# Kernel tuning notes

Measured on AMD Instinct MI355X. Metric: run time of the kernel, lower is better.

Reference implementation:

```python
import jax, jax.numpy as jnp
import numpy as np

B, S, DM, H, DK, DV = 2, 2048, 1024, 16, 64, 64

def setup_inputs() -> dict:
    key = jax.random.key(0)
    ks = jax.random.split(key, 12)
    s = 0.02
    return {
        "Q": jax.random.normal(ks[0], (B, S, DM), jnp.float32),
        "K": jax.random.normal(ks[1], (B, S, DM), jnp.float32),
        "V": jax.random.normal(ks[2], (B, S, DM), jnp.float32),
        "mask": jax.random.randint(ks[3], (B, S, S), 0, 2).astype(bool),
        "wq": jax.random.normal(ks[4], (DM, H * DK), jnp.float32) * s,
        "bq": jnp.zeros((H * DK,), jnp.float32),
        "wk": jax.random.normal(ks[5], (DM, H * DK), jnp.float32) * s,
        "bk": jnp.zeros((H * DK,), jnp.float32),
        "wv": jax.random.normal(ks[6], (DM, H * DV), jnp.float32) * s,
        "bv": jnp.zeros((H * DV,), jnp.float32),
        "wo": jax.random.normal(ks[7], (H * DV, DM), jnp.float32) * s,
        "bo": jnp.zeros((DM,), jnp.float32),
    }

def reference(Q, K, V, mask, wq, bq, wk, bk, wv, bv, wo, bo):
    b = Q.shape[0]
    # projections -> [b, h, s, d]
    q = (Q @ wq + bq).reshape(b, -1, H, DK).transpose(0, 2, 1, 3)
    k = (K @ wk + bk).reshape(b, -1, H, DK).transpose(0, 2, 1, 3)
    v = (V @ wv + bv).reshape(b, -1, H, DV).transpose(0, 2, 1, 3)
    # scaled dot-product attention with boolean mask (True = masked out)
    scores = jnp.einsum("bhqd,bhkd->bhqk", q, k) / jnp.sqrt(jnp.float32(DK))
    scores = jnp.where(mask[:, None, :, :], jnp.float32(-1e9), scores)
    attn = jax.nn.softmax(scores, axis=-1)  # [b,h,s,s]
    ctx = jnp.einsum("bhqk,bhkd->bhqd", attn, v)
    ctx = ctx.transpose(0, 2, 1, 3).reshape(b, -1, H * DV)
    out = ctx @ wo + bo  # [b, s, d_model]
    return out, attn
```

## Files before the change

### kernel.cpp

```cpp
#include <hip/hip_runtime.h>

typedef unsigned short u16;
typedef unsigned int u32;
typedef unsigned long long u64;
typedef __attribute__((ext_vector_type(8))) short bf16x8;
typedef __attribute__((ext_vector_type(4))) float f32x4;

#define NB 2
#define NS 2048
#define NDM 1024
#define NH 16

#define MFMA_B16(a, b, c) __builtin_amdgcn_mfma_f32_16x16x32_bf16(a, b, c, 0, 0, 0)

__device__ __forceinline__ u16 f2bf(float f) {
  union { float f; unsigned u; } v; v.f = f;
  return (u16)((v.u + 0x7fffu + ((v.u >> 16) & 1u)) >> 16);
}
__device__ __forceinline__ float bf2f(u16 h) {
  union { float f; unsigned u; } v; v.u = ((u32)h) << 16; return v.f;
}

__global__ __launch_bounds__(256) void cast3_bf16(const float* __restrict__ a,
                                                  const float* __restrict__ b,
                                                  const float* __restrict__ c,
                                                  u16* __restrict__ oa, u16* __restrict__ ob,
                                                  u16* __restrict__ oc) {
  int i = blockIdx.x * 256 + threadIdx.x;
  const float* src; u16* dst; int j;
  if (i < 1048576) { src = a; dst = oa; j = i; }
  else if (i < 2097152) { src = b; dst = ob; j = i - 1048576; }
  else { src = c; dst = oc; j = i - 2097152; }
  const float4 v = reinterpret_cast<const float4*>(src)[j];
  ushort4 o; o.x = f2bf(v.x); o.y = f2bf(v.y); o.z = f2bf(v.z); o.w = f2bf(v.w);
  reinterpret_cast<ushort4*>(dst)[j] = o;
}

struct TW4 { const float* in[4]; u16* out[4]; };
__global__ __launch_bounds__(256) void transpose_w4(TW4 tw) {
  __shared__ float tile[32][33];
  const float* in = tw.in[blockIdx.z];
  u16* out = tw.out[blockIdx.z];
  int bx = blockIdx.x, by = blockIdx.y;
  int x = threadIdx.x & 31, y0 = threadIdx.x >> 5;
#pragma unroll
  for (int i = 0; i < 4; i++) {
    int y = y0 + i * 8;
    tile[y][x] = in[(by * 32 + y) * NDM + bx * 32 + x];
  }
  __syncthreads();
#pragma unroll
  for (int i = 0; i < 4; i++) {
    int y = y0 + i * 8;
    out[(bx * 32 + y) * NDM + by * 32 + x] = f2bf(tile[x][y]);
  }
}

__global__ __launch_bounds__(256) void mask2bits(const u32* __restrict__ mask, u32* __restrict__ mb) {
  int idx = blockIdx.x * 256 + threadIdx.x;
  u32 mw0 = mask[threadIdx.x & 63];
  bool floatmode = (__ballot(mw0 == 0x3F800000u) != 0ull);
  bool bytemode = !floatmode && (__ballot((mw0 >> 8) != 0u) != 0ull);
  int row = idx >> 6;
  int wword = idx & 63;
  u32 bits = 0;
  if (!bytemode) {
    const uint4* p = reinterpret_cast<const uint4*>(mask + (size_t)row * 2048 + wword * 32);
#pragma unroll
    for (int i = 0; i < 8; i++) {
      uint4 v = p[i];
      bits |= (v.x ? 1u : 0u) << (i * 4 + 0);
      bits |= (v.y ? 1u : 0u) << (i * 4 + 1);
      bits |= (v.z ? 1u : 0u) << (i * 4 + 2);
      bits |= (v.w ? 1u : 0u) << (i * 4 + 3);
    }
  } else {
    const uint4* p = reinterpret_cast<const uint4*>(
        reinterpret_cast<const unsigned char*>(mask) + (size_t)row * 2048 + wword * 32);
#pragma unroll
    for (int i = 0; i < 2; i++) {
      uint4 v = p[i];
      u32 wsv[4] = {v.x, v.y, v.z, v.w};
#pragma unroll
      for (int j = 0; j < 4; j++)
#pragma unroll
        for (int kq = 0; kq < 4; kq++)
          bits |= ((((wsv[j] >> (kq * 8)) & 0xffu) != 0u) ? 1u : 0u) << (i * 16 + j * 4 + kq);
    }
  }
  mb[idx] = bits;
}

struct GArgs { const u16* X; const u16* W; const float* bias; void* out; int mode; float scale; };

__global__ __launch_bounds__(256, 2) void gemm_bt(GArgs g0, GArgs g1, GArgs g2) {
  GArgs ga = (blockIdx.z == 0) ? g0 : (blockIdx.z == 1 ? g1 : g2);
  const int K = 1024, N = 1024;
  __shared__ u16 As[128 * 32];
  __shared__ u16 Bs[128 * 32];
  const int t = threadIdx.x, w = t >> 6, l = t & 63;
  const int m0 = blockIdx.x * 128, n0 = blockIdx.y * 128;
  const int wm = (w >> 1) * 64, wn = (w & 1) * 64;
  const f32x4 fz = {0.f, 0.f, 0.f, 0.f};
  f32x4 acc[4][4];
#pragma unroll
  for (int i = 0; i < 4; i++)
#pragma unroll
    for (int j = 0; j < 4; j++) acc[i][j] = fz;

  for (int k0 = 0; k0 < K; k0 += 32) {
#pragma unroll
    for (int i = 0; i < 2; i++) {
      int idx = i * 256 + w * 64 + l;
      int r = idx >> 2, c = (idx & 3) * 8;
      __builtin_amdgcn_global_load_lds(
          reinterpret_cast<const unsigned*>(ga.X + (size_t)(m0 + r) * K + k0 + c),
          reinterpret_cast<unsigned*>(&As[(i * 256 + w * 64) * 8]), 16, 0, 0);
      __builtin_amdgcn_global_load_lds(
          reinterpret_cast<const unsigned*>(ga.W + (size_t)(n0 + r) * K + k0 + c),
          reinterpret_cast<unsigned*>(&Bs[(i * 256 + w * 64) * 8]), 16, 0, 0);
    }
    __syncthreads();
    bf16x8 af[4], bfr[4];
#pragma unroll
    for (int mt = 0; mt < 4; mt++)
      af[mt] = *reinterpret_cast<const bf16x8*>(&As[(wm + mt * 16 + (l & 15)) * 32 + (l >> 4) * 8]);
#pragma unroll
    for (int nt = 0; nt < 4; nt++)
      bfr[nt] = *reinterpret_cast<const bf16x8*>(&Bs[(wn + nt * 16 + (l & 15)) * 32 + (l >> 4) * 8]);
#pragma unroll
    for (int mt = 0; mt < 4; mt++)
#pragma unroll
      for (int nt = 0; nt < 4; nt++)
        acc[mt][nt] = MFMA_B16(af[mt], bfr[nt], acc[mt][nt]);
    __syncthreads();
  }

#pragma unroll
  for (int nt = 0; nt < 4; nt++) {
    int n = n0 + wn + nt * 16 + (l & 15);
    float bias = ga.bias[n];
#pragma unroll
    for (int mt = 0; mt < 4; mt++) {
      int mb = m0 + wm + mt * 16 + ((l >> 4) << 2);
#pragma unroll
      for (int r = 0; r < 4; r++) {
        int m = mb + r;
        float v = (acc[mt][nt][r] + bias) * ga.scale;
        if (ga.mode == 2) {
          reinterpret_cast<float*>(ga.out)[(size_t)m * N + n] = v;
        } else {
          int b = m >> 11, s = m & 2047, h = n >> 6, d = n & 63;
          if (ga.mode == 0)
            reinterpret_cast<u16*>(ga.out)[(((size_t)(b * NH + h) * NS + s) << 6) + d] = f2bf(v);
          else
            reinterpret_cast<u16*>(ga.out)[((size_t)(b * NH + h) * 64 + d) * NS + s] = f2bf(v);
        }
      }
    }
  }
}

__global__ __launch_bounds__(256, 4) void attn_kernel(
    const u16* __restrict__ qh, const u16* __restrict__ kh, const u16* __restrict__ vT,
    const u32* __restrict__ mb, float* __restrict__ attn, u16* __restrict__ ctx) {
  __shared__ u16 Ks[2][32 * 64];
  __shared__ u16 Vs[2][64 * 32];
  __shared__ u16 Ps[4][16 * 40];
  const int tid = threadIdx.x, w = tid >> 6, l = tid & 63;
  int id = blockIdx.x;
  int wgid = (id & 7) * 128 + (id >> 3);
  int qt = wgid & 31, pr = wgid >> 5;
  int h = pr & 15, b = pr >> 4;
  const size_t head = (size_t)b * NH + h;
  const u16* qp = qh + head * NS * 64;
  const u16* kp = kh + head * NS * 64;
  const u16* vp = vT + head * 64 * NS;
  const int qr0 = qt * 64 + w * 16;
  const int lo = l & 15, hi = l >> 4;
  const int rbase = hi << 2;
  const f32x4 fz = {0.f, 0.f, 0.f, 0.f};

  bf16x8 aq0, aq1;
  {
    const u16* p = qp + (size_t)(qr0 + lo) * 64 + hi * 8;
    aq0 = *reinterpret_cast<const bf16x8*>(p);
    aq1 = *reinterpret_cast<const bf16x8*>(p + 32);
  }
  const u32* mrow = mb + ((size_t)b * NS + qr0 + rbase) * 64;

  const int k_row = tid >> 3, k_slot = tid & 7;
  const u16* ksrc0 = kp + (size_t)k_row * 64 + ((k_slot ^ (k_row & 7)) * 8);
  const int v_dv = tid >> 2, v_slot = tid & 3;
  const u16* vsrc0 = vp + (size_t)v_dv * NS + ((v_slot ^ ((v_dv >> 1) & 3)) * 8);
  const int sxk = lo & 7;
  const int sxv = (lo >> 1) & 3;

#define STAGE_KT(tt)                                                                    \
  __builtin_amdgcn_global_load_lds(                                                     \
      reinterpret_cast<const unsigned*>(ksrc0 + (size_t)(tt) * 2048),                   \
      reinterpret_cast<unsigned*>(&Ks[(tt) & 1][w * 512]), 16, 0, 0);
#define STAGE_VT(tt)                                                                    \
  __builtin_amdgcn_global_load_lds(                                                     \
      reinterpret_cast<const unsigned*>(vsrc0 + (size_t)(tt) * 32),                     \
      reinterpret_cast<unsigned*>(&Vs[(tt) & 1][w * 512]), 16, 0, 0);

  float rs0 = 0.f, rs1 = 0.f, rs2 = 0.f, rs3 = 0.f;

  u32 mc0 = mrow[0], mc1 = mrow[64], mc2 = mrow[128], mc3 = mrow[192];
  STAGE_KT(0);
  asm volatile("s_waitcnt vmcnt(0)" ::: "memory");
  __builtin_amdgcn_s_barrier();
  asm volatile("" ::: "memory");

  for (int t = 0; t < 64; ++t) {
    STAGE_KT(t + 1);
    u32 mn0 = mrow[t + 1], mn1 = mrow[65 + t], mn2 = mrow[129 + t], mn3 = mrow[193 + t];
    asm volatile("" ::: "memory");
    const u16* kbase = &Ks[t & 1][0];
    bf16x8 b00 = *reinterpret_cast<const bf16x8*>(&kbase[(lo) * 64 + ((hi ^ sxk) * 8)]);
    bf16x8 b01 = *reinterpret_cast<const bf16x8*>(&kbase[(lo) * 64 + (((4 + hi) ^ sxk) * 8)]);
    bf16x8 b10 = *reinterpret_cast<const bf16x8*>(&kbase[(16 + lo) * 64 + ((hi ^ sxk) * 8)]);
    bf16x8 b11 = *reinterpret_cast<const bf16x8*>(&kbase[(16 + lo) * 64 + (((4 + hi) ^ sxk) * 8)]);
    f32x4 s0 = MFMA_B16(aq1, b01, MFMA_B16(aq0, b00, fz));
    f32x4 s1 = MFMA_B16(aq1, b11, MFMA_B16(aq0, b10, fz));
    rs0 += ((mc0 >> lo) & 1u) ? 0.f : __expf(s0[0]);
    rs1 += ((mc1 >> lo) & 1u) ? 0.f : __expf(s0[1]);
    rs2 += ((mc2 >> lo) & 1u) ? 0.f : __expf(s0[2]);
    rs3 += ((mc3 >> lo) & 1u) ? 0.f : __expf(s0[3]);
    int bit1 = 16 + lo;
    rs0 += ((mc0 >> bit1) & 1u) ? 0.f : __expf(s1[0]);
    rs1 += ((mc1 >> bit1) & 1u) ? 0.f : __expf(s1[1]);
    rs2 += ((mc2 >> bit1) & 1u) ? 0.f : __expf(s1[2]);
    rs3 += ((mc3 >> bit1) & 1u) ? 0.f : __expf(s1[3]);
    mc0 = mn0; mc1 = mn1; mc2 = mn2; mc3 = mn3;
    asm volatile("s_waitcnt vmcnt(4)" ::: "memory");
    __builtin_amdgcn_s_barrier();
    asm volatile("" ::: "memory");
  }

  {
    float v;
    v = rs0; v += __shfl_xor(v, 1); v += __shfl_xor(v, 2); v += __shfl_xor(v, 4); v += __shfl_xor(v, 8);
    rs0 = 1.f / fmaxf(v, 1e-30f);
    v = rs1; v += __shfl_xor(v, 1); v += __shfl_xor(v, 2); v += __shfl_xor(v, 4); v += __shfl_xor(v, 8);
    rs1 = 1.f / fmaxf(v, 1e-30f);
    v = rs2; v += __shfl_xor(v, 1); v += __shfl_xor(v, 2); v += __shfl_xor(v, 4); v += __shfl_xor(v, 8);
    rs2 = 1.f / fmaxf(v, 1e-30f);
    v = rs3; v += __shfl_xor(v, 1); v += __shfl_xor(v, 2); v += __shfl_xor(v, 4); v += __shfl_xor(v, 8);
    rs3 = 1.f / fmaxf(v, 1e-30f);
  }

  f32x4 c0 = fz, c1 = fz, c2 = fz, c3 = fz;
  float* abase = attn + (head * NS + qr0) * NS;
  u16* psw = &Ps[w][0];
  const int srow = l >> 2, schunk = l & 3;

  mc0 = mrow[0]; mc1 = mrow[64]; mc2 = mrow[128]; mc3 = mrow[192];
  STAGE_KT(0);
  STAGE_VT(0);
  asm volatile("s_waitcnt vmcnt(0)" ::: "memory");
  __builtin_amdgcn_s_barrier();
  asm volatile("" ::: "memory");

  for (int t = 0; t < 64; ++t) {
    STAGE_KT(t + 1);
    STAGE_VT(t + 1);
    u32 mn0 = mrow[t + 1], mn1 = mrow[65 + t], mn2 = mrow[129 + t], mn3 = mrow[193 + t];
    asm volatile("" ::: "memory");
    const u16* kbase = &Ks[t & 1][0];
    const u16* vbase = &Vs[t & 1][0];
    bf16x8 b00 = *reinterpret_cast<const bf16x8*>(&kbase[(lo) * 64 + ((hi ^ sxk) * 8)]);
    bf16x8 b01 = *reinterpret_cast<const bf16x8*>(&kbase[(lo) * 64 + (((4 + hi) ^ sxk) * 8)]);
    bf16x8 b10 = *reinterpret_cast<const bf16x8*>(&kbase[(16 + lo) * 64 + ((hi ^ sxk) * 8)]);
    bf16x8 b11 = *reinterpret_cast<const bf16x8*>(&kbase[(16 + lo) * 64 + (((4 + hi) ^ sxk) * 8)]);
    f32x4 s0 = MFMA_B16(aq1, b01, MFMA_B16(aq0, b00, fz));
    f32x4 s1 = MFMA_B16(aq1, b11, MFMA_B16(aq0, b10, fz));
    float p;
    p = ((mc0 >> lo) & 1u) ? 0.f : __expf(s0[0]) * rs0; psw[(rbase + 0) * 40 + lo] = f2bf(p);
    p = ((mc1 >> lo) & 1u) ? 0.f : __expf(s0[1]) * rs1; psw[(rbase + 1) * 40 + lo] = f2bf(p);
    p = ((mc2 >> lo) & 1u) ? 0.f : __expf(s0[2]) * rs2; psw[(rbase + 2) * 40 + lo] = f2bf(p);
    p = ((mc3 >> lo) & 1u) ? 0.f : __expf(s0[3]) * rs3; psw[(rbase + 3) * 40 + lo] = f2bf(p);
    int bit1 = 16 + lo;
    p = ((mc0 >> bit1) & 1u) ? 0.f : __expf(s1[0]) * rs0; psw[(rbase + 0) * 40 + 16 + lo] = f2bf(p);
    p = ((mc1 >> bit1) & 1u) ? 0.f : __expf(s1[1]) * rs1; psw[(rbase + 1) * 40 + 16 + lo] = f2bf(p);
    p = ((mc2 >> bit1) & 1u) ? 0.f : __expf(s1[2]) * rs2; psw[(rbase + 2) * 40 + 16 + lo] = f2bf(p);
    p = ((mc3 >> bit1) & 1u) ? 0.f : __expf(s1[3]) * rs3; psw[(rbase + 3) * 40 + 16 + lo] = f2bf(p);
    mc0 = mn0; mc1 = mn1; mc2 = mn2; mc3 = mn3;
    {
      bf16x8 pa = *reinterpret_cast<const bf16x8*>(&psw[lo * 40 + hi * 8]);
      bf16x8 v0 = *reinterpret_cast<const bf16x8*>(&vbase[(lo) * 32 + ((hi ^ sxv) * 8)]);
      bf16x8 v1 = *reinterpret_cast<const bf16x8*>(&vbase[(16 + lo) * 32 + ((hi ^ sxv) * 8)]);
      bf16x8 v2 = *reinterpret_cast<const bf16x8*>(&vbase[(32 + lo) * 32 + ((hi ^ sxv) * 8)]);
      bf16x8 v3 = *reinterpret_cast<const bf16x8*>(&vbase[(48 + lo) * 32 + ((hi ^ sxv) * 8)]);
      c0 = MFMA_B16(pa, v0, c0);
      c1 = MFMA_B16(pa, v1, c1);
      c2 = MFMA_B16(pa, v2, c2);
      c3 = MFMA_B16(pa, v3, c3);
    }
    {
      float* arow = abase + (size_t)srow * NS + t * 32 + schunk * 8;
      bf16x8 q0 = *reinterpret_cast<const bf16x8*>(&psw[srow * 40 + schunk * 8]);
      f32x4 o0, o1;
#pragma unroll
      for (int j = 0; j < 4; ++j) { o0[j] = bf2f((u16)q0[j]); o1[j] = bf2f((u16)q0[j + 4]); }
      *reinterpret_cast<f32x4*>(arow + 0) = o0;
      *reinterpret_cast<f32x4*>(arow + 4) = o1;
    }
    asm volatile("s_waitcnt vmcnt(6)" ::: "memory");
    __builtin_amdgcn_s_barrier();
    asm volatile("" ::: "memory");
  }

#define CTXW(cv, ct)                                                                      \
  {                                                                                       \
    ctx[((size_t)b * NS + qr0 + rbase + 0) * 1024 + h * 64 + (ct)*16 + lo] = f2bf(cv[0]); \
    ctx[((size_t)b * NS + qr0 + rbase + 1) * 1024 + h * 64 + (ct)*16 + lo] = f2bf(cv[1]); \
    ctx[((size_t)b * NS + qr0 + rbase + 2) * 1024 + h * 64 + (ct)*16 + lo] = f2bf(cv[2]); \
    ctx[((size_t)b * NS + qr0 + rbase + 3) * 1024 + h * 64 + (ct)*16 + lo] = f2bf(cv[3]); \
  }
  CTXW(c0, 0) CTXW(c1, 1) CTXW(c2, 2) CTXW(c3, 3)
#undef CTXW
#undef STAGE_KT
#undef STAGE_VT
}

extern "C" void kernel_launch(void* const* d_in, const int* in_sizes, int n_in,
                              void* d_out, int out_size, void* d_ws, size_t ws_size,
                              hipStream_t stream) {
  const float* Q = (const float*)d_in[0];
  const float* K = (const float*)d_in[1];
  const float* V = (const float*)d_in[2];
  const u32* mask = (const u32*)d_in[3];
  const float* wq = (const float*)d_in[4];
  const float* bq = (const float*)d_in[5];
  const float* wk = (const float*)d_in[6];
  const float* bk = (const float*)d_in[7];
  const float* wv = (const float*)d_in[8];
  const float* bv = (const float*)d_in[9];
  const float* wo = (const float*)d_in[10];
  const float* bo = (const float*)d_in[11];
  float* out = (float*)d_out;
  float* attn = out + (size_t)NB * NS * NDM;

  char* ws = (char*)d_ws;
  u16* Qb  = (u16*)(ws + 0);
  u16* Kb  = (u16*)(ws + 8388608);
  u16* Vb  = (u16*)(ws + 16777216);
  u16* wqT = (u16*)(ws + 25165824);
  u16* wkT = (u16*)(ws + 27262976);
  u16* wvT = (u16*)(ws + 29360128);
  u16* woT = (u16*)(ws + 31457280);
  u16* qhd = (u16*)(ws + 33554432);
  u16* khd = (u16*)(ws + 41943040);
  u16* vTd = (u16*)(ws + 50331648);
  u16* ctx = (u16*)(ws + 58720256);
  u32* mbits = (u32*)(ws + 0);

  cast3_bf16<<<12288, 256, 0, stream>>>(Q, K, V, Qb, Kb, Vb);
  TW4 tw;
  tw.in[0] = wq; tw.in[1] = wk; tw.in[2] = wv; tw.in[3] = wo;
  tw.out[0] = wqT; tw.out[1] = wkT; tw.out[2] = wvT; tw.out[3] = woT;
  transpose_w4<<<dim3(32, 32, 4), 256, 0, stream>>>(tw);

  GArgs gq = {Qb, wqT, bq, (void*)qhd, 0, 0.125f};
  GArgs gk = {Kb, wkT, bk, (void*)khd, 0, 1.0f};
  GArgs gv = {Vb, wvT, bv, (void*)vTd, 1, 1.0f};
  gemm_bt<<<dim3(32, 8, 3), 256, 0, stream>>>(gq, gk, gv);

  mask2bits<<<1024, 256, 0, stream>>>(mask, mbits);

  attn_kernel<<<1024, 256, 0, stream>>>(qhd, khd, vTd, mbits, attn, ctx);

  GArgs go = {ctx, woT, bo, d_out, 2, 1.0f};
  gemm_bt<<<dim3(32, 8, 1), 256, 0, stream>>>(go, go, go);
}
```

Baseline: 334.9 us.

## Software-pipeline attention loop so PV of previous tile overlaps next QK

Restructures the second pass of the attention kernel so each iteration runs the P·V MFMAs and attention-probability stores for tile t-1 while computing QK and exp for tile t. To make this safe it adds a prologue and epilogue, triple-buffers the V tile in LDS and double-buffers each wave's P scratch. The aim is to hide MFMA and LDS latency behind the exp work and global stores. The cost is more LDS use and higher register pressure, which could lower occupancy.

```diff
diff --git a/kernel.cpp b/kernel.cpp
--- a/kernel.cpp
+++ b/kernel.cpp
@@ -165,8 +165,8 @@
     const u16* __restrict__ qh, const u16* __restrict__ kh, const u16* __restrict__ vT,
     const u32* __restrict__ mb, float* __restrict__ attn, u16* __restrict__ ctx) {
   __shared__ u16 Ks[2][32 * 64];
-  __shared__ u16 Vs[2][64 * 32];
-  __shared__ u16 Ps[4][16 * 40];
+  __shared__ u16 Vs[3][64 * 32];
+  __shared__ u16 Ps[4][2][16 * 40];
   const int tid = threadIdx.x, w = tid >> 6, l = tid & 63;
   int id = blockIdx.x;
   int wgid = (id & 7) * 128 + (id >> 3);
@@ -196,34 +196,76 @@
   const int sxk = lo & 7;
   const int sxv = (lo >> 1) & 3;
 
-#define STAGE_KT(tt)                                                                    \
+#define STAGE_KT(tt, bi)                                                                \
   __builtin_amdgcn_global_load_lds(                                                     \
       reinterpret_cast<const unsigned*>(ksrc0 + (size_t)(tt) * 2048),                   \
-      reinterpret_cast<unsigned*>(&Ks[(tt) & 1][w * 512]), 16, 0, 0);
-#define STAGE_VT(tt)                                                                    \
+      reinterpret_cast<unsigned*>(&Ks[bi][w * 512]), 16, 0, 0);
+#define STAGE_VT(tt, bi)                                                                \
   __builtin_amdgcn_global_load_lds(                                                     \
       reinterpret_cast<const unsigned*>(vsrc0 + (size_t)(tt) * 32),                     \
-      reinterpret_cast<unsigned*>(&Vs[(tt) & 1][w * 512]), 16, 0, 0);
+      reinterpret_cast<unsigned*>(&Vs[bi][w * 512]), 16, 0, 0);
+
+#define QK_TILE(kb, s0, s1)                                                             \
+  {                                                                                     \
+    const u16* kbase = &Ks[kb][0];                                                      \
+    bf16x8 b00 = *reinterpret_cast<const bf16x8*>(&kbase[(lo) * 64 + ((hi ^ sxk) * 8)]);        \
+    bf16x8 b01 = *reinterpret_cast<const bf16x8*>(&kbase[(lo) * 64 + (((4 + hi) ^ sxk) * 8)]);  \
+    bf16x8 b10 = *reinterpret_cast<const bf16x8*>(&kbase[(16 + lo) * 64 + ((hi ^ sxk) * 8)]);   \
+    bf16x8 b11 = *reinterpret_cast<const bf16x8*>(&kbase[(16 + lo) * 64 + (((4 + hi) ^ sxk) * 8)]); \
+    s0 = MFMA_B16(aq1, b01, MFMA_B16(aq0, b00, fz));                                    \
+    s1 = MFMA_B16(aq1, b11, MFMA_B16(aq0, b10, fz));                                    \
+  }
+#define EXP_PS(pb, s0, s1)                                                              \
+  {                                                                                     \
+    u16* pc = &Ps[w][pb][0];                                                            \
+    float p;                                                                            \
+    p = ((mc0 >> lo) & 1u) ? 0.f : __expf(s0[0]) * rs0; pc[(rbase + 0) * 40 + lo] = f2bf(p); \
+    p = ((mc1 >> lo) & 1u) ? 0.f : __expf(s0[1]) * rs1; pc[(rbase + 1) * 40 + lo] = f2bf(p); \
+    p = ((mc2 >> lo) & 1u) ? 0.f : __expf(s0[2]) * rs2; pc[(rbase + 2) * 40 + lo] = f2bf(p); \
+    p = ((mc3 >> lo) & 1u) ? 0.f : __expf(s0[3]) * rs3; pc[(rbase + 3) * 40 + lo] = f2bf(p); \
+    int bit1 = 16 + lo;                                                                 \
+    p = ((mc0 >> bit1) & 1u) ? 0.f : __expf(s1[0]) * rs0; pc[(rbase + 0) * 40 + 16 + lo] = f2bf(p); \
+    p = ((mc1 >> bit1) & 1u) ? 0.f : __expf(s1[1]) * rs1; pc[(rbase + 1) * 40 + 16 + lo] = f2bf(p); \
+    p = ((mc2 >> bit1) & 1u) ? 0.f : __expf(s1[2]) * rs2; pc[(rbase + 2) * 40 + 16 + lo] = f2bf(p); \
+    p = ((mc3 >> bit1) & 1u) ? 0.f : __expf(s1[3]) * rs3; pc[(rbase + 3) * 40 + 16 + lo] = f2bf(p); \
+  }
+#define PV_STORES(tt, pb, vb)                                                           \
+  {                                                                                     \
+    u16* pp = &Ps[w][pb][0];                                                            \
+    const u16* vbase = &Vs[vb][0];                                                      \
+    bf16x8 pa = *reinterpret_cast<const bf16x8*>(&pp[lo * 40 + hi * 8]);                \
+    bf16x8 v0 = *reinterpret_cast<const bf16x8*>(&vbase[(lo) * 32 + ((hi ^ sxv) * 8)]);        \
+    bf16x8 v1 = *reinterpret_cast<const bf16x8*>(&vbase[(16 + lo) * 32 + ((hi ^ sxv) * 8)]);   \
+    bf16x8 v2 = *reinterpret_cast<const bf16x8*>(&vbase[(32 + lo) * 32 + ((hi ^ sxv) * 8)]);   \
+    bf16x8 v3 = *reinterpret_cast<const bf16x8*>(&vbase[(48 + lo) * 32 + ((hi ^ sxv) * 8)]);   \
+    c0 = MFMA_B16(pa, v0, c0);                                                          \
+    c1 = MFMA_B16(pa, v1, c1);                                                          \
+    c2 = MFMA_B16(pa, v2, c2);                                                          \
+    c3 = MFMA_B16(pa, v3, c3);                                                          \
+    float* arow = abase + (size_t)srow * NS + (tt) * 32 + schunk * 8;                   \
+    bf16x8 q0 = *reinterpret_cast<const bf16x8*>(&pp[srow * 40 + schunk * 8]);          \
+    f32x4 o0, o1;                                                                       \
+    _Pragma("unroll") for (int j = 0; j < 4; ++j) {                                     \
+      o0[j] = bf2f((u16)q0[j]); o1[j] = bf2f((u16)q0[j + 4]);                           \
+    }                                                                                   \
+    *reinterpret_cast<f32x4*>(arow + 0) = o0;                                           \
+    *reinterpret_cast<f32x4*>(arow + 4) = o1;                                           \
+  }
 
   float rs0 = 0.f, rs1 = 0.f, rs2 = 0.f, rs3 = 0.f;
 
   u32 mc0 = mrow[0], mc1 = mrow[64], mc2 = mrow[128], mc3 = mrow[192];
-  STAGE_KT(0);
+  STAGE_KT(0, 0);
   asm volatile("s_waitcnt vmcnt(0)" ::: "memory");
   __builtin_amdgcn_s_barrier();
   asm volatile("" ::: "memory");
 
   for (int t = 0; t < 64; ++t) {
-    STAGE_KT(t + 1);
+    STAGE_KT(t + 1, (t + 1) & 1);
     u32 mn0 = mrow[t + 1], mn1 = mrow[65 + t], mn2 = mrow[129 + t], mn3 = mrow[193 + t];
     asm volatile("" ::: "memory");
-    const u16* kbase = &Ks[t & 1][0];
-    bf16x8 b00 = *reinterpret_cast<const bf16x8*>(&kbase[(lo) * 64 + ((hi ^ sxk) * 8)]);
-    bf16x8 b01 = *reinterpret_cast<const bf16x8*>(&kbase[(lo) * 64 + (((4 + hi) ^ sxk) * 8)]);
-    bf16x8 b10 = *reinterpret_cast<const bf16x8*>(&kbase[(16 + lo) * 64 + ((hi ^ sxk) * 8)]);
-    bf16x8 b11 = *reinterpret_cast<const bf16x8*>(&kbase[(16 + lo) * 64 + (((4 + hi) ^ sxk) * 8)]);
-    f32x4 s0 = MFMA_B16(aq1, b01, MFMA_B16(aq0, b00, fz));
-    f32x4 s1 = MFMA_B16(aq1, b11, MFMA_B16(aq0, b10, fz));
+    f32x4 s0, s1;
+    QK_TILE(t & 1, s0, s1);
     rs0 += ((mc0 >> lo) & 1u) ? 0.f : __expf(s0[0]);
     rs1 += ((mc1 >> lo) & 1u) ? 0.f : __expf(s0[1]);
     rs2 += ((mc2 >> lo) & 1u) ? 0.f : __expf(s0[2]);
@@ -253,64 +295,48 @@
 
   f32x4 c0 = fz, c1 = fz, c2 = fz, c3 = fz;
   float* abase = attn + (head * NS + qr0) * NS;
-  u16* psw = &Ps[w][0];
   const int srow = l >> 2, schunk = l & 3;
 
   mc0 = mrow[0]; mc1 = mrow[64]; mc2 = mrow[128]; mc3 = mrow[192];
-  STAGE_KT(0);
-  STAGE_VT(0);
+  STAGE_KT(0, 0);
+  STAGE_VT(0, 0);
   asm volatile("s_waitcnt vmcnt(0)" ::: "memory");
   __builtin_amdgcn_s_barrier();
   asm volatile("" ::: "memory");
 
-  for (int t = 0; t < 64; ++t) {
-    STAGE_KT(t + 1);
-    STAGE_VT(t + 1);
+  {
+    STAGE_KT(1, 1);
+    STAGE_VT(1, 1);
+    u32 mn0 = mrow[1], mn1 = mrow[65], mn2 = mrow[129], mn3 = mrow[193];
+    asm volatile("" ::: "memory");
+    f32x4 s0, s1;
+    QK_TILE(0, s0, s1);
+    EXP_PS(0, s0, s1);
+    mc0 = mn0; mc1 = mn1; mc2 = mn2; mc3 = mn3;
+    asm volatile("s_waitcnt vmcnt(4)" ::: "memory");
+    __builtin_amdgcn_s_barrier();
+    asm volatile("" ::: "memory");
+  }
+
+  for (int t = 1; t < 64; ++t) {
+    if (t + 1 < 64) {
+      int vb2 = (t + 1) % 3;
+      STAGE_KT(t + 1, (t + 1) & 1);
+      STAGE_VT(t + 1, vb2);
+    }
     u32 mn0 = mrow[t + 1], mn1 = mrow[65 + t], mn2 = mrow[129 + t], mn3 = mrow[193 + t];
     asm volatile("" ::: "memory");
-    const u16* kbase = &Ks[t & 1][0];
-    const u16* vbase = &Vs[t & 1][0];
-    bf16x8 b00 = *reinterpret_cast<const bf16x8*>(&kbase[(lo) * 64 + ((hi ^ sxk) * 8)]);
-    bf16x8 b01 = *reinterpret_cast<const bf16x8*>(&kbase[(lo) * 64 + (((4 + hi) ^ sxk) * 8)]);
-    bf16x8 b10 = *reinterpret_cast<const bf16x8*>(&kbase[(16 + lo) * 64 + ((hi ^ sxk) * 8)]);
-    bf16x8 b11 = *reinterpret_cast<const bf16x8*>(&kbase[(16 + lo) * 64 + (((4 + hi) ^ sxk) * 8)]);
-    f32x4 s0 = MFMA_B16(aq1, b01, MFMA_B16(aq0, b00, fz));
-    f32x4 s1 = MFMA_B16(aq1, b11, MFMA_B16(aq0, b10, fz));
-    float p;
-    p = ((mc0 >> lo) & 1u) ? 0.f : __expf(s0[0]) * rs0; psw[(rbase + 0) * 40 + lo] = f2bf(p);
-    p = ((mc1 >> lo) & 1u) ? 0.f : __expf(s0[1]) * rs1; psw[(rbase + 1) * 40 + lo] = f2bf(p);
-    p = ((mc2 >> lo) & 1u) ? 0.f : __expf(s0[2]) * rs2; psw[(rbase + 2) * 40 + lo] = f2bf(p);
-    p = ((mc3 >> lo) & 1u) ? 0.f : __expf(s0[3]) * rs3; psw[(rbase + 3) * 40 + lo] = f2bf(p);
-    int bit1 = 16 + lo;
-    p = ((mc0 >> bit1) & 1u) ? 0.f : __expf(s1[0]) * rs0; psw[(rbase + 0) * 40 + 16 + lo] = f2bf(p);
-    p = ((mc1 >> bit1) & 1u) ? 0.f : __expf(s1[1]) * rs1; psw[(rbase + 1) * 40 + 16 + lo] = f2bf(p);
-    p = ((mc2 >> bit1) & 1u) ? 0.f : __expf(s1[2]) * rs2; psw[(rbase + 2) * 40 + 16 + lo] = f2bf(p);
-    p = ((mc3 >> bit1) & 1u) ? 0.f : __expf(s1[3]) * rs3; psw[(rbase + 3) * 40 + 16 + lo] = f2bf(p);
+    PV_STORES(t - 1, (t - 1) & 1, (t - 1) % 3);
+    f32x4 s0, s1;
+    QK_TILE(t & 1, s0, s1);
+    EXP_PS(t & 1, s0, s1);
     mc0 = mn0; mc1 = mn1; mc2 = mn2; mc3 = mn3;
-    {
-      bf16x8 pa = *reinterpret_cast<const bf16x8*>(&psw[lo * 40 + hi * 8]);
-      bf16x8 v0 = *reinterpret_cast<const bf16x8*>(&vbase[(lo) * 32 + ((hi ^ sxv) * 8)]);
-      bf16x8 v1 = *reinterpret_cast<const bf16x8*>(&vbase[(16 + lo) * 32 + ((hi ^ sxv) * 8)]);
-      bf16x8 v2 = *reinterpret_cast<const bf16x8*>(&vbase[(32 + lo) * 32 + ((hi ^ sxv) * 8)]);
-      bf16x8 v3 = *reinterpret_cast<const bf16x8*>(&vbase[(48 + lo) * 32 + ((hi ^ sxv) * 8)]);
-      c0 = MFMA_B16(pa, v0, c0);
-      c1 = MFMA_B16(pa, v1, c1);
-      c2 = MFMA_B16(pa, v2, c2);
-      c3 = MFMA_B16(pa, v3, c3);
-    }
-    {
-      float* arow = abase + (size_t)srow * NS + t * 32 + schunk * 8;
-      bf16x8 q0 = *reinterpret_cast<const bf16x8*>(&psw[srow * 40 + schunk * 8]);
-      f32x4 o0, o1;
-#pragma unroll
-      for (int j = 0; j < 4; ++j) { o0[j] = bf2f((u16)q0[j]); o1[j] = bf2f((u16)q0[j + 4]); }
-      *reinterpret_cast<f32x4*>(arow + 0) = o0;
-      *reinterpret_cast<f32x4*>(arow + 4) = o1;
-    }
     asm volatile("s_waitcnt vmcnt(6)" ::: "memory");
     __builtin_amdgcn_s_barrier();
     asm volatile("" ::: "memory");
   }
+
+  PV_STORES(63, 1, 0);
 
 #define CTXW(cv, ct)                                                                      \
   {                                                                                       \
@@ -323,6 +349,9 @@
 #undef CTXW
 #undef STAGE_KT
 #undef STAGE_VT
+#undef QK_TILE
+#undef EXP_PS
+#undef PV_STORES
 }
 
 extern "C" void kernel_launch(void* const* d_in, const int* in_sizes, int n_in,
```

After: 330.4 us (median of 2 runs). Within noise of the previous version (-1.3%).
